# Optimization experiments

Hardware: AMD Instinct MI355X
Metric: run time of the kernel (lower is better)

Reference implementation:

```python
import jax, jax.numpy as jnp
import numpy as np

B, T, F_IN, F_OUT = 16, 2048, 128, 128
ALPHA = 0.2  # LeakyReLU negative slope
MASK_VAL = -1e9


def setup_inputs() -> dict:
    key = jax.random.key(0)
    kx, kw, ka, kadj = jax.random.split(key, 4)
    # xavier_uniform-ish scale for W and a (gain=1.414)
    w_bound = 1.414 * np.sqrt(6.0 / (F_IN + F_OUT))
    a_bound = 1.414 * np.sqrt(6.0 / (2 * F_OUT + 1))
    x = jax.random.normal(kx, (B, T, F_IN), jnp.float32)
    W = jax.random.uniform(kw, (F_IN, F_OUT), jnp.float32, -w_bound, w_bound)
    a = jax.random.uniform(ka, (2 * F_OUT, 1), jnp.float32, -a_bound, a_bound)
    adj = jax.random.randint(kadj, (B, T, T), 0, 2, jnp.int32)
    return {"x": x, "adj": adj, "W": W, "a": a}


def reference(x, adj, W, a):
    # h: [B,T,F_OUT]
    h = jnp.einsum('btf,fo->bto', x, W)
    # Additive GAT score decomposition: e[b,i,j] = leakyrelu(h_i . a1 + h_j . a2)
    # Mathematically identical to cat([h_i,h_j]) @ a, without the BxTxTx2F tensor.
    a1 = a[:F_OUT, 0]   # [F_OUT]
    a2 = a[F_OUT:, 0]   # [F_OUT]
    s1 = h @ a1         # [B,T]
    s2 = h @ a2         # [B,T]
    e = jax.nn.leaky_relu(s1[:, :, None] + s2[:, None, :], ALPHA)  # [B,T,T]
    e = jnp.where(adj == 0, MASK_VAL, e)
    att = jax.nn.softmax(e, axis=-1)  # [B,T,T]
    # dropout=0.0 / eval mode -> identity
    return att @ h  # [B,T,F_OUT]
```

## Files before the change

### kernel.cpp

```cpp
#include <hip/hip_runtime.h>
#include <hip/hip_bf16.h>

#define TT 2048
#define NB 16
#define FD 128
#define ALPHA 0.2f

typedef __attribute__((ext_vector_type(8))) short short8;
typedef __attribute__((ext_vector_type(4))) float f32x4;
typedef __attribute__((ext_vector_type(16))) float f32x16;

static __device__ __forceinline__ unsigned short f2bf(float f) {
    unsigned u = __float_as_uint(f);
    u += 0x7FFF + ((u >> 16) & 1);
    return (unsigned short)(u >> 16);
}
static __device__ __forceinline__ unsigned short bfbits(float f) {
    return __builtin_bit_cast(unsigned short, __float2bfloat16(f));
}

__global__ __launch_bounds__(256) void k_wt(const float* __restrict__ W,
                                            unsigned short* __restrict__ WT)
{
    int fid = blockIdx.x * 256 + threadIdx.x;
    int k = fid >> 5;
    int f = (fid & 31) << 2;
    float4 w4 = *reinterpret_cast<const float4*>(W + k * FD + f);
    WT[(f + 0) * FD + k] = f2bf(w4.x);
    WT[(f + 1) * FD + k] = f2bf(w4.y);
    WT[(f + 2) * FD + k] = f2bf(w4.z);
    WT[(f + 3) * FD + k] = f2bf(w4.w);
}

__global__ __launch_bounds__(256, 8) void k_prep(const float* __restrict__ x,
                                                 const unsigned short* __restrict__ WT,
                                                 const float* __restrict__ a,
                                                 const int* __restrict__ adj,
                                                 unsigned short* __restrict__ hF,
                                                 float* __restrict__ s1,
                                                 float* __restrict__ s2,
                                                 unsigned char* __restrict__ bm)
{
    __shared__ unsigned short hs[128][72];

    const int tid = threadIdx.x;
    const int w = tid >> 6, l = tid & 63;

    if (blockIdx.x >= 512) {
        const int row = (blockIdx.x - 512) * 4 + w;
        const int* ap = adj + (size_t)row * TT;
        unsigned char* op = bm + (size_t)row * 256;

        #pragma unroll
        for (int rd = 0; rd < 8; ++rd) {
            int4 q = *reinterpret_cast<const int4*>(ap + rd * 256 + l * 4);
            unsigned long long m0 = __ballot(q.x != 0);
            unsigned long long m1 = __ballot(q.y != 0);
            unsigned long long m2 = __ballot(q.z != 0);
            unsigned long long m3 = __ballot(q.w != 0);
            if (l < 32) {
                unsigned b =
                     ((unsigned)(m0 >> (2 * l)) & 1)
                  | (((unsigned)(m1 >> (2 * l)) & 1) << 1)
                  | (((unsigned)(m2 >> (2 * l)) & 1) << 2)
                  | (((unsigned)(m3 >> (2 * l)) & 1) << 3)
                  | (((unsigned)(m0 >> (2 * l + 1)) & 1) << 4)
                  | (((unsigned)(m1 >> (2 * l + 1)) & 1) << 5)
                  | (((unsigned)(m2 >> (2 * l + 1)) & 1) << 6)
                  | (((unsigned)(m3 >> (2 * l + 1)) & 1) << 7);
                op[rd * 32 + l] = (unsigned char)b;
            }
        }
        return;
    }

    const int b  = blockIdx.x >> 5;
    const int t0 = (blockIdx.x & 31) << 6;
    const int g = l >> 4, r15 = l & 15;

    const float* xrow = x + ((size_t)(b * TT + t0 + w * 16 + r15)) * FD;

    f32x4 acc[8] = {};

    #pragma unroll
    for (int m = 0; m < 4; ++m) {
        const int koff = m * 32 + g * 8;
        float4 xa = *reinterpret_cast<const float4*>(xrow + koff);
        float4 xb = *reinterpret_cast<const float4*>(xrow + koff + 4);
        short8 af;
        af[0] = (short)f2bf(xa.x); af[1] = (short)f2bf(xa.y);
        af[2] = (short)f2bf(xa.z); af[3] = (short)f2bf(xa.w);
        af[4] = (short)f2bf(xb.x); af[5] = (short)f2bf(xb.y);
        af[6] = (short)f2bf(xb.z); af[7] = (short)f2bf(xb.w);
        #pragma unroll
        for (int n = 0; n < 8; ++n) {
            short8 bfr = *reinterpret_cast<const short8*>(WT + (n * 16 + r15) * FD + koff);
            acc[n] = __builtin_amdgcn_mfma_f32_16x16x32_bf16(af, bfr, acc[n], 0, 0, 0);
        }
    }

    float p1[4] = {0.f, 0.f, 0.f, 0.f}, p2[4] = {0.f, 0.f, 0.f, 0.f};
    #pragma unroll
    for (int n = 0; n < 8; ++n) {
        float a1v = a[n * 16 + r15];
        float a2v = a[FD + n * 16 + r15];
        #pragma unroll
        for (int r = 0; r < 4; ++r) {
            p1[r] += acc[n][r] * a1v;
            p2[r] += acc[n][r] * a2v;
        }
    }
    #pragma unroll
    for (int r = 0; r < 4; ++r) {
        #pragma unroll
        for (int off = 8; off >= 1; off >>= 1) {
            p1[r] += __shfl_xor(p1[r], off);
            p2[r] += __shfl_xor(p2[r], off);
        }
    }
    if (r15 == 0) {
        const int trow = t0 + w * 16 + g * 4;
        #pragma unroll
        for (int r = 0; r < 4; ++r) {
            s1[b * TT + trow + r] = p1[r];
            s2[b * TT + trow + r] = p2[r];
        }
    }

    #pragma unroll
    for (int n = 0; n < 8; ++n)
        #pragma unroll
        for (int r = 0; r < 4; ++r)
            hs[n * 16 + r15][w * 16 + g * 4 + r] = f2bf(acc[n][r]);
    __syncthreads();

    #pragma unroll
    for (int it = 0; it < 4; ++it) {
        int idx = it * 256 + tid;
        int lp = idx & 63;
        int frag = idx >> 6;
        int n32 = frag & 3, tl = frag >> 2;
        int fsrc = n32 * 32 + (lp & 31);
        int tsrc = tl * 16 + (lp >> 5) * 8;
        short8 v = *reinterpret_cast<const short8*>(&hs[fsrc][tsrc]);
        *reinterpret_cast<short8*>(
            hF + (((size_t)(b * 128 + (t0 >> 4) + tl)) * 4 + n32) * 512 + lp * 8) = v;
    }
}

__global__ __launch_bounds__(256, 4) void k_att(const unsigned char* __restrict__ bm,
                                                const unsigned short* __restrict__ hF,
                                                const float* __restrict__ s1,
                                                const float* __restrict__ s2,
                                                float* __restrict__ out)
{
    __shared__ __align__(16) float red[2][32][132];
    __shared__ float dsum[4][32];

    const int tid = threadIdx.x;
    const int wg = (blockIdx.x & 7) * 128 + (blockIdx.x >> 3);
    const int b  = wg >> 6;
    const int i0 = (wg & 63) << 5;
    const int w = tid >> 6, l = tid & 63;
    const int il = l & 31, h = l >> 5;
    const int hsh = h * 8;

    const int jbeg = w * (TT / 4);
    const float s1v = s1[b * TT + i0 + il];
    const float* s2p = s2 + b * TT + jbeg + h * 8;
    const unsigned char* bmrow = bm + ((size_t)(b * TT + i0 + il)) * 256 + w * 64;
    const unsigned short* hfp = hF + ((size_t)(b * 128 + (jbeg >> 4))) * 4 * 512 + l * 8;

    f32x16 acc[4] = {};
    float rsum = 0.f;

    short8 bb[2][4];
    #pragma unroll
    for (int n = 0; n < 4; ++n)
        bb[0][n] = *reinterpret_cast<const short8*>(hfp + (size_t)n * 512);

    uint4 bq;

    #pragma unroll
    for (int t = 0; t < 32; ++t) {
        const int cur = t & 1;
        if (t < 31) {
            #pragma unroll
            for (int n = 0; n < 4; ++n)
                bb[cur ^ 1][n] = *reinterpret_cast<const short8*>(
                    hfp + (size_t)((t + 1) * 4 + n) * 512);
        }
        if ((t & 7) == 0)
            bq = *reinterpret_cast<const uint4*>(bmrow + (t >> 3) * 16);
        const int wi = (t & 7) >> 1;
        const unsigned wsel = wi == 0 ? bq.x : wi == 1 ? bq.y : wi == 2 ? bq.z : bq.w;
        const unsigned bits = (wsel >> ((t & 1) * 16 + hsh)) & 0xffu;

        float4 sa = *reinterpret_cast<const float4*>(s2p + t * 16);
        float4 sb = *reinterpret_cast<const float4*>(s2p + t * 16 + 4);
        float csf[8] = {sa.x, sa.y, sa.z, sa.w, sb.x, sb.y, sb.z, sb.w};
        float pv[8];
        #pragma unroll
        for (int e = 0; e < 8; ++e) {
            float s = s1v + csf[e];
            s = fmaxf(s, ALPHA * s);
            float p = ((int)(bits << (31 - e)) < 0) ? __expf(s) : 0.f;
            rsum += p;
            pv[e] = p;
        }
        short8 af;
        #pragma unroll
        for (int e = 0; e < 8; ++e)
            af[e] = (short)bfbits(pv[e]);
        #pragma unroll
        for (int n = 0; n < 4; ++n)
            acc[n] = __builtin_amdgcn_mfma_f32_32x32x16_bf16(af, bb[cur][n], acc[n], 0, 0, 0);
    }

    rsum += __shfl_xor(rsum, 32);
    if (l < 32) dsum[w][l] = rsum;

    if (w < 2) {
        #pragma unroll
        for (int n = 0; n < 4; ++n)
            #pragma unroll
            for (int r = 0; r < 16; ++r) {
                int irow = (r & 3) + 8 * (r >> 2) + 4 * h;
                red[w][irow][n * 32 + il] = acc[n][r];
            }
    }
    __syncthreads();
    if (w >= 2) {
        #pragma unroll
        for (int n = 0; n < 4; ++n)
            #pragma unroll
            for (int r = 0; r < 16; ++r) {
                int irow = (r & 3) + 8 * (r >> 2) + 4 * h;
                red[w - 2][irow][n * 32 + il] += acc[n][r];
            }
    }
    __syncthreads();

    #pragma unroll
    for (int it = 0; it < 4; ++it) {
        int e = it * 256 + tid;
        int row = e >> 5;
        int c4 = (e & 31) << 2;
        float4 v0 = *reinterpret_cast<const float4*>(&red[0][row][c4]);
        float4 v1 = *reinterpret_cast<const float4*>(&red[1][row][c4]);
        float dn = dsum[0][row] + dsum[1][row] + dsum[2][row] + dsum[3][row];
        float ri = 1.0f / dn;
        float4 o;
        o.x = (v0.x + v1.x) * ri;
        o.y = (v0.y + v1.y) * ri;
        o.z = (v0.z + v1.z) * ri;
        o.w = (v0.w + v1.w) * ri;
        *reinterpret_cast<float4*>(out + ((size_t)(b * TT + i0 + row)) * FD + c4) = o;
    }
}

extern "C" void kernel_launch(void* const* d_in, const int* in_sizes, int n_in,
                              void* d_out, int out_size, void* d_ws, size_t ws_size,
                              hipStream_t stream)
{
    const float* x  = (const float*)d_in[0];
    const int* adj  = (const int*)d_in[1];
    const float* W  = (const float*)d_in[2];
    const float* a  = (const float*)d_in[3];
    float* out = (float*)d_out;

    unsigned short* hF = (unsigned short*)d_ws;
    float* s1 = (float*)((char*)d_ws + (size_t)NB * FD * TT * 2);
    float* s2 = s1 + NB * TT;
    unsigned short* WT = (unsigned short*)(s2 + NB * TT);
    unsigned char* bm = (unsigned char*)(WT + FD * FD);

    k_wt  <<<16, 256, 0, stream>>>(W, WT);
    k_prep<<<512 + NB * TT / 4, 256, 0, stream>>>(x, WT, a, adj, hF, s1, s2, bm);
    k_att <<<NB * (TT / 32), 256, 0, stream>>>(bm, hF, s1, s2, out);
}
```

Measured before the change: 104.6 us.

## Read int32 adjacency directly in attention kernel instead of prepacked bitmask

Removes the adjacency bit-packing pass from the prep kernel and has the attention kernel load int32 adj values directly, double-buffered alongside the h fragments. This drops a separate full read of adj plus a bitmask write and re-read. In exchange, each attention thread streams 32x more mask bytes inside the hot loop, uses more registers (occupancy hint lowered from 4 to 3), and adj is read once per row block with less compact transfers.

```diff
diff --git a/kernel.cpp b/kernel.cpp
--- a/kernel.cpp
+++ b/kernel.cpp
@@ -32,51 +32,19 @@
     WT[(f + 3) * FD + k] = f2bf(w4.w);
 }
 
-__global__ __launch_bounds__(256, 8) void k_prep(const float* __restrict__ x,
-                                                 const unsigned short* __restrict__ WT,
-                                                 const float* __restrict__ a,
-                                                 const int* __restrict__ adj,
-                                                 unsigned short* __restrict__ hF,
-                                                 float* __restrict__ s1,
-                                                 float* __restrict__ s2,
-                                                 unsigned char* __restrict__ bm)
+__global__ __launch_bounds__(256) void k_h(const float* __restrict__ x,
+                                           const unsigned short* __restrict__ WT,
+                                           const float* __restrict__ a,
+                                           unsigned short* __restrict__ hF,
+                                           float* __restrict__ s1,
+                                           float* __restrict__ s2)
 {
     __shared__ unsigned short hs[128][72];
 
     const int tid = threadIdx.x;
-    const int w = tid >> 6, l = tid & 63;
-
-    if (blockIdx.x >= 512) {
-        const int row = (blockIdx.x - 512) * 4 + w;
-        const int* ap = adj + (size_t)row * TT;
-        unsigned char* op = bm + (size_t)row * 256;
-
-        #pragma unroll
-        for (int rd = 0; rd < 8; ++rd) {
-            int4 q = *reinterpret_cast<const int4*>(ap + rd * 256 + l * 4);
-            unsigned long long m0 = __ballot(q.x != 0);
-            unsigned long long m1 = __ballot(q.y != 0);
-            unsigned long long m2 = __ballot(q.z != 0);
-            unsigned long long m3 = __ballot(q.w != 0);
-            if (l < 32) {
-                unsigned b =
-                     ((unsigned)(m0 >> (2 * l)) & 1)
-                  | (((unsigned)(m1 >> (2 * l)) & 1) << 1)
-                  | (((unsigned)(m2 >> (2 * l)) & 1) << 2)
-                  | (((unsigned)(m3 >> (2 * l)) & 1) << 3)
-                  | (((unsigned)(m0 >> (2 * l + 1)) & 1) << 4)
-                  | (((unsigned)(m1 >> (2 * l + 1)) & 1) << 5)
-                  | (((unsigned)(m2 >> (2 * l + 1)) & 1) << 6)
-                  | (((unsigned)(m3 >> (2 * l + 1)) & 1) << 7);
-                op[rd * 32 + l] = (unsigned char)b;
-            }
-        }
-        return;
-    }
-
     const int b  = blockIdx.x >> 5;
     const int t0 = (blockIdx.x & 31) << 6;
-    const int g = l >> 4, r15 = l & 15;
+    const int w = tid >> 6, l = tid & 63, g = l >> 4, r15 = l & 15;
 
     const float* xrow = x + ((size_t)(b * TT + t0 + w * 16 + r15)) * FD;
 
@@ -148,7 +116,7 @@
     }
 }
 
-__global__ __launch_bounds__(256, 4) void k_att(const unsigned char* __restrict__ bm,
+__global__ __launch_bounds__(256, 3) void k_att(const int* __restrict__ adj,
                                                 const unsigned short* __restrict__ hF,
                                                 const float* __restrict__ s1,
                                                 const float* __restrict__ s2,
@@ -163,12 +131,11 @@
     const int i0 = (wg & 63) << 5;
     const int w = tid >> 6, l = tid & 63;
     const int il = l & 31, h = l >> 5;
-    const int hsh = h * 8;
 
     const int jbeg = w * (TT / 4);
     const float s1v = s1[b * TT + i0 + il];
     const float* s2p = s2 + b * TT + jbeg + h * 8;
-    const unsigned char* bmrow = bm + ((size_t)(b * TT + i0 + il)) * 256 + w * 64;
+    const int* adjp = adj + ((size_t)(b * TT + i0 + il)) * TT + jbeg + h * 8;
     const unsigned short* hfp = hF + ((size_t)(b * 128 + (jbeg >> 4))) * 4 * 512 + l * 8;
 
     f32x16 acc[4] = {};
@@ -179,32 +146,33 @@
     for (int n = 0; n < 4; ++n)
         bb[0][n] = *reinterpret_cast<const short8*>(hfp + (size_t)n * 512);
 
-    uint4 bq;
+    int4 ar[2][2];
+    ar[0][0] = *reinterpret_cast<const int4*>(adjp);
+    ar[0][1] = *reinterpret_cast<const int4*>(adjp + 4);
 
     #pragma unroll
     for (int t = 0; t < 32; ++t) {
         const int cur = t & 1;
         if (t < 31) {
+            ar[cur ^ 1][0] = *reinterpret_cast<const int4*>(adjp + (t + 1) * 16);
+            ar[cur ^ 1][1] = *reinterpret_cast<const int4*>(adjp + (t + 1) * 16 + 4);
             #pragma unroll
             for (int n = 0; n < 4; ++n)
                 bb[cur ^ 1][n] = *reinterpret_cast<const short8*>(
                     hfp + (size_t)((t + 1) * 4 + n) * 512);
         }
-        if ((t & 7) == 0)
-            bq = *reinterpret_cast<const uint4*>(bmrow + (t >> 3) * 16);
-        const int wi = (t & 7) >> 1;
-        const unsigned wsel = wi == 0 ? bq.x : wi == 1 ? bq.y : wi == 2 ? bq.z : bq.w;
-        const unsigned bits = (wsel >> ((t & 1) * 16 + hsh)) & 0xffu;
 
         float4 sa = *reinterpret_cast<const float4*>(s2p + t * 16);
         float4 sb = *reinterpret_cast<const float4*>(s2p + t * 16 + 4);
         float csf[8] = {sa.x, sa.y, sa.z, sa.w, sb.x, sb.y, sb.z, sb.w};
+        const int ad[8] = {ar[cur][0].x, ar[cur][0].y, ar[cur][0].z, ar[cur][0].w,
+                           ar[cur][1].x, ar[cur][1].y, ar[cur][1].z, ar[cur][1].w};
         float pv[8];
         #pragma unroll
         for (int e = 0; e < 8; ++e) {
             float s = s1v + csf[e];
             s = fmaxf(s, ALPHA * s);
-            float p = ((int)(bits << (31 - e)) < 0) ? __expf(s) : 0.f;
+            float p = ad[e] ? __expf(s) : 0.f;
             rsum += p;
             pv[e] = p;
         }
@@ -273,9 +241,8 @@
     float* s1 = (float*)((char*)d_ws + (size_t)NB * FD * TT * 2);
     float* s2 = s1 + NB * TT;
     unsigned short* WT = (unsigned short*)(s2 + NB * TT);
-    unsigned char* bm = (unsigned char*)(WT + FD * FD);
-
-    k_wt  <<<16, 256, 0, stream>>>(W, WT);
-    k_prep<<<512 + NB * TT / 4, 256, 0, stream>>>(x, WT, a, adj, hF, s1, s2, bm);
-    k_att <<<NB * (TT / 32), 256, 0, stream>>>(bm, hF, s1, s2, out);
-}
+
+    k_wt <<<16, 256, 0, stream>>>(W, WT);
+    k_h  <<<NB * (TT / 64), 256, 0, stream>>>(x, WT, a, hF, s1, s2);
+    k_att<<<NB * (TT / 32), 256, 0, stream>>>(adj, hF, s1, s2, out);
+}
```

Measured after the change: 117.3 us. 12.1% more time.
